# Kernel tuning notes

Hardware: AMD Instinct MI355X
Metric: run time of the kernel (lower is better)

The kernel has to match this reference:

```python
import jax, jax.numpy as jnp
import numpy as np

B, S, E, H = 2, 2048, 768, 8
D = E // H  # 96
SCALING = D ** (-0.5)


def setup_inputs() -> dict:
    key = jax.random.key(0)
    ks = jax.random.split(key, 7)
    sd = E ** -0.5
    return {
        "x": jax.random.normal(ks[0], (B, S, E), jnp.float32),
        "Wq": jax.random.normal(ks[1], (E, E), jnp.float32) * sd,
        "bq": jax.random.normal(ks[2], (E,), jnp.float32) * 0.02,
        "Wk": jax.random.normal(ks[3], (E, E), jnp.float32) * sd,
        "bk": jax.random.normal(ks[4], (E,), jnp.float32) * 0.02,
        "Wo": jax.random.normal(ks[5], (E, E), jnp.float32) * sd,
        "bo": jax.random.normal(ks[6], (E,), jnp.float32) * 0.02,
    }


def _split_heads(t):
    # [B, S, E] -> [B, H, S, D]
    return t.reshape(B, S, H, D).transpose(0, 2, 1, 3)


def reference(x, Wq, bq, Wk, bk, Wo, bo):
    q = _split_heads(x @ Wq + bq)
    k = _split_heads(x @ Wk + bk)
    # NOTE: faithful to source bug — values use the KEY projection
    v = _split_heads(x @ Wk + bk)
    energies = jnp.einsum("bhqd,bhkd->bhqk", q, k)  # [B,H,S,S]
    # NOTE: faithful to source — scaling applied AFTER softmax
    attn = jax.nn.softmax(energies, axis=-1) * SCALING
    out = jnp.einsum("bhqk,bhkd->bhqd", attn, v)
    out = out.transpose(0, 2, 1, 3).reshape(B, S, E)
    return out @ Wo + bo
```

## Files before the change

### kernel.cpp

```cpp
#include <hip/hip_runtime.h>
#include <hip/hip_bf16.h>
#include <math.h>
#include <stdint.h>

#define B_DIM 2
#define S_DIM 2048
#define E_DIM 768
#define H_DIM 8
#define D_DIM 96
#define M_DIM (B_DIM*S_DIM)
#define SCALE_F 0.10206207261596575f
#define LOG2E_F 1.44269504088896341f

typedef _Float16 f16x8 __attribute__((ext_vector_type(8)));
typedef float    f32x4  __attribute__((ext_vector_type(4)));
typedef float    f32x16 __attribute__((ext_vector_type(16)));
typedef unsigned int u32x4 __attribute__((ext_vector_type(4)));

#define MFMA16H(a,b,c) __builtin_amdgcn_mfma_f32_16x16x32_f16(a,b,c,0,0,0)
#define MFMA32H(a,b,c) __builtin_amdgcn_mfma_f32_32x32x16_f16(a,b,c,0,0,0)

__device__ inline unsigned short f2h(float f) {
    return __builtin_bit_cast(unsigned short, (_Float16)f);
}

__device__ inline unsigned pk2(float a, float b) {
    return __builtin_bit_cast(unsigned, __builtin_amdgcn_cvt_pkrtz(a, b));
}

__device__ inline void gload16(const void* g, void* l) {
    auto gp = reinterpret_cast<const __attribute__((address_space(1))) uint32_t*>(
        reinterpret_cast<uintptr_t>(g));
    auto lp = reinterpret_cast<__attribute__((address_space(3))) uint32_t*>(
        reinterpret_cast<uintptr_t>(l));
    __builtin_amdgcn_global_load_lds(gp, lp, 16, 0, 0);
}

__global__ __launch_bounds__(256) void prep_kernel(
    const float* __restrict__ X,
    const float* __restrict__ W0, const float* __restrict__ W1,
    const float* __restrict__ W2,
    unsigned short* __restrict__ Xf,
    unsigned short* __restrict__ T0, unsigned short* __restrict__ T1,
    unsigned short* __restrict__ T2)
{
    const int tid = threadIdx.x;
    if (blockIdx.x < 3072) {
        int i = (blockIdx.x * 256 + tid) * 4;
        float4 v = *(const float4*)(X + i);
        ushort4 h;
        h.x = f2h(v.x); h.y = f2h(v.y); h.z = f2h(v.z); h.w = f2h(v.w);
        *(ushort4*)(Xf + i) = h;
        return;
    }
    int idx = blockIdx.x - 3072;
    int z = idx / 144, rem = idx % 144;
    const float* W; unsigned short* T;
    if (z == 0)      { W = W0; T = T0; }
    else if (z == 1) { W = W1; T = T1; }
    else             { W = W2; T = T2; }
    const float sc = (z == 0) ? LOG2E_F : 1.0f;
    int k0 = (rem / 12) << 6, n0 = (rem % 12) << 6;

    __shared__ float tile[64][65];
    const int r = tid >> 4, c4 = (tid & 15) << 2;
    #pragma unroll
    for (int i = 0; i < 4; ++i) {
        float4 v = *(const float4*)(W + (size_t)(k0 + r + i*16)*E_DIM + n0 + c4);
        tile[r + i*16][c4+0] = v.x; tile[r + i*16][c4+1] = v.y;
        tile[r + i*16][c4+2] = v.z; tile[r + i*16][c4+3] = v.w;
    }
    __syncthreads();
    #pragma unroll
    for (int i = 0; i < 4; ++i) {
        int n = r + i*16;
        ushort4 h;
        h.x = f2h(tile[c4+0][n] * sc); h.y = f2h(tile[c4+1][n] * sc);
        h.z = f2h(tile[c4+2][n] * sc); h.w = f2h(tile[c4+3][n] * sc);
        *(ushort4*)(T + (size_t)(n0 + n)*E_DIM + k0 + c4) = h;
    }
}

__global__ __launch_bounds__(256) void gemm_qk_kernel(
    const unsigned short* __restrict__ A, const unsigned short* __restrict__ Bt,
    const float* __restrict__ bq, const float* __restrict__ bk,
    unsigned short* __restrict__ Qf, unsigned short* __restrict__ Kf)
{
    __shared__ unsigned short sA[2*128*32];
    __shared__ unsigned short sB[2*64*32];

    const int tid  = threadIdx.x;
    const int lane = tid & 63;
    const int w    = tid >> 6;
    const int qn   = lane & 15, quad = lane >> 4;
    const int wm   = w & 1, wn = w >> 1;

    const int flat = blockIdx.x;
    const int g = flat & 7, s = flat >> 3;
    const int row0 = ((g << 2) + (s & 3)) << 7;
    const int col0 = (s >> 2) << 6;

    const int ar = tid >> 2;
    const int ak = (tid & 3) << 3;

    const unsigned short* gA = A  + (size_t)(row0 + ar)*E_DIM + ak;
    const unsigned short* gB = Bt + (size_t)(col0 + ar)*E_DIM + ak;

    f32x4 acc[4][2];
    #pragma unroll
    for (int mt = 0; mt < 4; ++mt)
        #pragma unroll
        for (int nt = 0; nt < 2; ++nt)
            { acc[mt][nt][0]=0.f; acc[mt][nt][1]=0.f; acc[mt][nt][2]=0.f; acc[mt][nt][3]=0.f; }

    for (int k0 = 0; k0 < E_DIM; k0 += 64) {
        __syncthreads();
        gload16(gA + k0,                 sA + tid*8);
        gload16(gA + 64*E_DIM + k0,      sA + 2048 + tid*8);
        gload16(gA + k0 + 32,            sA + 4096 + tid*8);
        gload16(gA + 64*E_DIM + k0 + 32, sA + 6144 + tid*8);
        gload16(gB + k0,                 sB + tid*8);
        gload16(gB + k0 + 32,            sB + 2048 + tid*8);
        __syncthreads();

        #pragma unroll
        for (int kk = 0; kk < 2; ++kk) {
            f16x8 af[4], bf[2];
            #pragma unroll
            for (int mt = 0; mt < 4; ++mt)
                af[mt] = *(const f16x8*)&sA[kk*4096 + (wm*64 + mt*16 + qn)*32 + quad*8];
            #pragma unroll
            for (int nt = 0; nt < 2; ++nt)
                bf[nt] = *(const f16x8*)&sB[kk*2048 + (wn*32 + nt*16 + qn)*32 + quad*8];
            #pragma unroll
            for (int mt = 0; mt < 4; ++mt)
                #pragma unroll
                for (int nt = 0; nt < 2; ++nt)
                    acc[mt][nt] = MFMA16H(af[mt], bf[nt], acc[mt][nt]);
        }
    }

    #pragma unroll
    for (int nt = 0; nt < 2; ++nt) {
        int n = col0 + wn*32 + nt*16 + qn;
        bool isQ = n < E_DIM;
        float bias = isQ ? bq[n] * LOG2E_F : bk[n - E_DIM];
        unsigned short* op = isQ ? Qf : Kf;
        int nc = isQ ? n : n - E_DIM;
        #pragma unroll
        for (int mt = 0; mt < 4; ++mt)
            #pragma unroll
            for (int r = 0; r < 4; ++r) {
                int m = row0 + wm*64 + mt*16 + quad*4 + r;
                op[(size_t)m*E_DIM + nc] = f2h(acc[mt][nt][r] + bias);
            }
    }
}

__global__ __launch_bounds__(256, 3) void attn_mfma_kernel(
    const unsigned short* __restrict__ Qf, const unsigned short* __restrict__ Kf,
    unsigned short* __restrict__ O0, unsigned short* __restrict__ O1,
    unsigned short* __restrict__ O2, unsigned short* __restrict__ O3,
    float2* __restrict__ ml)
{
    __shared__ unsigned short sKh[64][104];
    __shared__ unsigned short sKt[96][72];

    const int tid  = threadIdx.x;
    const int w    = tid >> 6;
    const int lane = tid & 63;
    const int col  = lane & 31;
    const int half = lane >> 5;
    const int b    = blockIdx.z >> 2;
    const int ks   = blockIdx.z & 3;
    const int h    = blockIdx.y;
    const int q0   = blockIdx.x << 7;
    const int key0 = ks << 9;

    f16x8 qf[6];
    {
        const size_t ro = ((size_t)(b*S_DIM + q0 + w*32 + col))*E_DIM
                          + h*D_DIM + half*8;
        #pragma unroll
        for (int kc = 0; kc < 6; ++kc)
            qf[kc] = *(const f16x8*)(Qf + ro + kc*16);
    }

    f32x16 o[3];
    #pragma unroll
    for (int nt = 0; nt < 3; ++nt)
        #pragma unroll
        for (int r = 0; r < 16; ++r) o[nt][r] = 0.f;
    float m_i = -INFINITY, l_i = 0.f;

    const bool stager = tid < 128;
    const int st = tid & 127;
    const int sp = st >> 2;
    const int dq = st & 3;
    const int kp2 = ((sp + ((dq & 1) << 4)) & 31) << 1;

    uint4 r0[3], r1[3];
    if (stager) {
        const size_t g0 = ((size_t)(b*S_DIM + key0 + 2*sp))*E_DIM + h*D_DIM + dq*8;
        #pragma unroll
        for (int i = 0; i < 3; ++i) {
            r0[i] = *(const uint4*)(Kf + g0 + 32*i);
            r1[i] = *(const uint4*)(Kf + g0 + E_DIM + 32*i);
        }
    }

    const int kswz = ((col >> 3) & 1) << 2;

    for (int kt = 0; kt < 8; ++kt) {
        if (stager) {
            #pragma unroll
            for (int i = 0; i < 3; ++i) {
                *(uint4*)&sKh[2*sp  ][dq*8 + 32*i] = r0[i];
                *(uint4*)&sKh[2*sp+1][dq*8 + 32*i] = r1[i];
            }
            const unsigned short* p0 = (const unsigned short*)r0;
            const unsigned short* p1 = (const unsigned short*)r1;
            #pragma unroll
            for (int c = 0; c < 24; ++c) {
                int d = dq*8 + ((c >> 3) << 5) + (c & 7);
                unsigned pk = (unsigned)p0[c] | ((unsigned)p1[c] << 16);
                *(unsigned*)&sKt[d][kp2] = pk;
            }
        }
        __syncthreads();

        if (stager && kt + 1 < 8) {
            const size_t g0 = ((size_t)(b*S_DIM + key0 + (kt+1)*64 + 2*sp))*E_DIM
                              + h*D_DIM + dq*8;
            #pragma unroll
            for (int i = 0; i < 3; ++i) {
                r0[i] = *(const uint4*)(Kf + g0 + 32*i);
                r1[i] = *(const uint4*)(Kf + g0 + E_DIM + 32*i);
            }
        }

        f32x16 s[2];
        #pragma unroll
        for (int mt = 0; mt < 2; ++mt) {
            f32x16 acc;
            #pragma unroll
            for (int r = 0; r < 16; ++r) acc[r] = 0.f;
            #pragma unroll
            for (int kc = 0; kc < 6; ++kc) {
                f16x8 ah = *(const f16x8*)&sKh[mt*32 + col][kc*16 + half*8];
                acc = MFMA32H(ah, qf[kc], acc);
            }
            s[mt] = acc;
        }

        float t[8];
        #pragma unroll
        for (int r = 0; r < 8; ++r)
            t[r] = fmaxf(fmaxf(s[0][r], s[0][r+8]), fmaxf(s[1][r], s[1][r+8]));
        float mx = fmaxf(fmaxf(fmaxf(t[0], t[1]), fmaxf(t[2], t[3])),
                         fmaxf(fmaxf(t[4], t[5]), fmaxf(t[6], t[7])));
        mx = fmaxf(mx, __shfl_xor(mx, 32));

        if (__any(mx > m_i + 10.0f)) {
            float m_new = fmaxf(m_i, mx);
            float alpha = __builtin_amdgcn_exp2f(m_i - m_new);
            l_i *= alpha;
            #pragma unroll
            for (int nt = 0; nt < 3; ++nt)
                #pragma unroll
                for (int r = 0; r < 16; ++r) o[nt][r] *= alpha;
            m_i = m_new;
        }

        #pragma unroll
        for (int mt = 0; mt < 2; ++mt)
            #pragma unroll
            for (int r = 0; r < 16; ++r)
                s[mt][r] = __builtin_amdgcn_exp2f(s[mt][r] - m_i);

        float a[8];
        #pragma unroll
        for (int r = 0; r < 8; ++r)
            a[r] = (s[0][r] + s[0][r+8]) + (s[1][r] + s[1][r+8]);
        float ps = ((a[0]+a[1]) + (a[2]+a[3])) + ((a[4]+a[5]) + (a[6]+a[7]));
        ps += __shfl_xor(ps, 32);
        l_i += ps;

        #pragma unroll
        for (int kc = 0; kc < 4; ++kc) {
            const int mt = kc >> 1;
            const int g0 = (kc & 1) << 3;
            unsigned A0 = pk2(s[mt][g0+0], s[mt][g0+1]);
            unsigned A1 = pk2(s[mt][g0+2], s[mt][g0+3]);
            unsigned B0 = pk2(s[mt][g0+4], s[mt][g0+5]);
            unsigned B1 = pk2(s[mt][g0+6], s[mt][g0+7]);
            auto w0 = __builtin_amdgcn_permlane32_swap(A0, B0, false, false);
            auto w1 = __builtin_amdgcn_permlane32_swap(A1, B1, false, false);
            u32x4 pw;
            pw[0] = w0[0]; pw[1] = w1[0]; pw[2] = w0[1]; pw[3] = w1[1];
            f16x8 pb = __builtin_bit_cast(f16x8, pw);
            #pragma unroll
            for (int nt = 0; nt < 3; ++nt) {
                f16x8 va = *(const f16x8*)
                    &sKt[nt*32 + col][(((kc << 1) | half) ^ kswz) << 3];
                o[nt] = MFMA32H(va, pb, o[nt]);
            }
        }
        __syncthreads();
    }

    float inv = 1.0f / l_i;
    unsigned short* Obase = O0;
    if (ks == 1) Obase = O1; else if (ks == 2) Obase = O2; else if (ks == 3) Obase = O3;
    unsigned short* Ob = Obase
        + ((size_t)(b*S_DIM + q0 + w*32 + col))*E_DIM + h*D_DIM;
    #pragma unroll
    for (int nt = 0; nt < 3; ++nt)
        #pragma unroll
        for (int rg = 0; rg < 4; ++rg) {
            ushort4 pk;
            pk.x = f2h(o[nt][4*rg+0]*inv); pk.y = f2h(o[nt][4*rg+1]*inv);
            pk.z = f2h(o[nt][4*rg+2]*inv); pk.w = f2h(o[nt][4*rg+3]*inv);
            *(ushort4*)(Ob + nt*32 + 8*rg + 4*half) = pk;
        }
    if (lane < 32) {
        int q = q0 + w*32 + lane;
        ml[((size_t)(ks*B_DIM + b)*H_DIM + h)*S_DIM + q] = make_float2(m_i, l_i);
    }
}

__device__ inline float4 mkscale4(const float2* __restrict__ ml, int m, int h) {
    int b = m >> 11, q = m & (S_DIM - 1);
    float2 e0 = ml[((size_t)(0*B_DIM + b)*H_DIM + h)*S_DIM + q];
    float2 e1 = ml[((size_t)(1*B_DIM + b)*H_DIM + h)*S_DIM + q];
    float2 e2 = ml[((size_t)(2*B_DIM + b)*H_DIM + h)*S_DIM + q];
    float2 e3 = ml[((size_t)(3*B_DIM + b)*H_DIM + h)*S_DIM + q];
    float mm = fmaxf(fmaxf(e0.x, e1.x), fmaxf(e2.x, e3.x));
    float w0 = e0.y * __builtin_amdgcn_exp2f(e0.x - mm);
    float w1 = e1.y * __builtin_amdgcn_exp2f(e1.x - mm);
    float w2 = e2.y * __builtin_amdgcn_exp2f(e2.x - mm);
    float w3 = e3.y * __builtin_amdgcn_exp2f(e3.x - mm);
    float inv = SCALE_F / (w0 + w1 + w2 + w3);
    return make_float4(w0*inv, w1*inv, w2*inv, w3*inv);
}

__global__ __launch_bounds__(256) void gemm_out_kernel(
    const unsigned short* __restrict__ O0, const unsigned short* __restrict__ O1,
    const unsigned short* __restrict__ O2, const unsigned short* __restrict__ O3,
    const float2* __restrict__ ml, const unsigned short* __restrict__ Bt,
    const float* __restrict__ bo, float* __restrict__ out)
{
    __shared__ unsigned short sA[2*64*32];
    __shared__ unsigned short sB[2*64*32];

    const int tid  = threadIdx.x;
    const int lane = tid & 63;
    const int w    = tid >> 6;
    const int qn   = lane & 15, quad = lane >> 4;
    const int wm   = w & 1, wn = w >> 1;

    const int flat = blockIdx.x;
    const int g = flat & 7, s = flat >> 3;
    const int row0 = ((g << 3) + (s & 7)) << 6;
    const int col0 = (s >> 3) << 6;

    const int ar = tid >> 2;
    const int ak = (tid & 3) << 3;

    const size_t r0o = (size_t)(row0 + ar)*E_DIM;
    const unsigned short* gB = Bt + (size_t)(col0 + ar)*E_DIM + ak;

    f32x4 acc[2][2];
    #pragma unroll
    for (int mt = 0; mt < 2; ++mt)
        #pragma unroll
        for (int nt = 0; nt < 2; ++nt)
            { acc[mt][nt][0]=0.f; acc[mt][nt][1]=0.f; acc[mt][nt][2]=0.f; acc[mt][nt][3]=0.f; }

    f16x8 u0A = *(const f16x8*)(O0 + r0o + ak);
    f16x8 u1A = *(const f16x8*)(O1 + r0o + ak);
    f16x8 u2A = *(const f16x8*)(O2 + r0o + ak);
    f16x8 u3A = *(const f16x8*)(O3 + r0o + ak);
    f16x8 u0B = *(const f16x8*)(O0 + r0o + 32 + ak);
    f16x8 u1B = *(const f16x8*)(O1 + r0o + 32 + ak);
    f16x8 u2B = *(const f16x8*)(O2 + r0o + 32 + ak);
    f16x8 u3B = *(const f16x8*)(O3 + r0o + 32 + ak);
    int hA = 0, hB = 0;
    float4 s4 = mkscale4(ml, row0 + ar, 0);
    _Float16 aA0 = (_Float16)s4.x, aA1 = (_Float16)s4.y;
    _Float16 aA2 = (_Float16)s4.z, aA3 = (_Float16)s4.w;
    _Float16 aB0 = aA0, aB1 = aA1, aB2 = aA2, aB3 = aA3;

    for (int k0 = 0; k0 < E_DIM; k0 += 64) {
        __syncthreads();
        {
            f16x8 c0 = (u0A*aA0 + u1A*aA1) + (u2A*aA2 + u3A*aA3);
            f16x8 c1 = (u0B*aB0 + u1B*aB1) + (u2B*aB2 + u3B*aB3);
            *(f16x8*)&sA[       ar*32 + ak] = c0;
            *(f16x8*)&sA[2048 + ar*32 + ak] = c1;
        }
        gload16(gB + k0,      sB + tid*8);
        gload16(gB + k0 + 32, sB + 2048 + tid*8);
        __syncthreads();

        if (k0 + 64 < E_DIM) {
            int kn = k0 + 64;
            u0A = *(const f16x8*)(O0 + r0o + kn + ak);
            u1A = *(const f16x8*)(O1 + r0o + kn + ak);
            u2A = *(const f16x8*)(O2 + r0o + kn + ak);
            u3A = *(const f16x8*)(O3 + r0o + kn + ak);
            u0B = *(const f16x8*)(O0 + r0o + kn + 32 + ak);
            u1B = *(const f16x8*)(O1 + r0o + kn + 32 + ak);
            u2B = *(const f16x8*)(O2 + r0o + kn + 32 + ak);
            u3B = *(const f16x8*)(O3 + r0o + kn + 32 + ak);
            int nhA = kn / D_DIM, nhB = (kn + 32) / D_DIM;
            if (nhA != hA) {
                float4 t4 = mkscale4(ml, row0 + ar, nhA);
                aA0 = (_Float16)t4.x; aA1 = (_Float16)t4.y;
                aA2 = (_Float16)t4.z; aA3 = (_Float16)t4.w; hA = nhA;
            }
            if (nhB != hB) {
                float4 t4 = mkscale4(ml, row0 + ar, nhB);
                aB0 = (_Float16)t4.x; aB1 = (_Float16)t4.y;
                aB2 = (_Float16)t4.z; aB3 = (_Float16)t4.w; hB = nhB;
            }
        }

        #pragma unroll
        for (int kk = 0; kk < 2; ++kk) {
            f16x8 af[2], bf[2];
            #pragma unroll
            for (int mt = 0; mt < 2; ++mt)
                af[mt] = *(const f16x8*)&sA[kk*2048 + (wm*32 + mt*16 + qn)*32 + quad*8];
            #pragma unroll
            for (int nt = 0; nt < 2; ++nt)
                bf[nt] = *(const f16x8*)&sB[kk*2048 + (wn*32 + nt*16 + qn)*32 + quad*8];
            #pragma unroll
            for (int mt = 0; mt < 2; ++mt)
                #pragma unroll
                for (int nt = 0; nt < 2; ++nt)
                    acc[mt][nt] = MFMA16H(af[mt], bf[nt], acc[mt][nt]);
        }
    }

    #pragma unroll
    for (int nt = 0; nt < 2; ++nt) {
        int n = col0 + wn*32 + nt*16 + qn;
        float bias = bo[n];
        #pragma unroll
        for (int mt = 0; mt < 2; ++mt)
            #pragma unroll
            for (int r = 0; r < 4; ++r) {
                int m = row0 + wm*32 + mt*16 + quad*4 + r;
                out[(size_t)m*E_DIM + n] = acc[mt][nt][r] + bias;
            }
    }
}

extern "C" void kernel_launch(void* const* d_in, const int* in_sizes, int n_in,
                              void* d_out, int out_size, void* d_ws, size_t ws_size,
                              hipStream_t stream)
{
    const float* x  = (const float*)d_in[0];
    const float* Wq = (const float*)d_in[1];
    const float* bq = (const float*)d_in[2];
    const float* Wk = (const float*)d_in[3];
    const float* bk = (const float*)d_in[4];
    const float* Wo = (const float*)d_in[5];
    const float* bo = (const float*)d_in[6];
    float* out = (float*)d_out;

    const size_t NE = (size_t)M_DIM * E_DIM;
    const size_t WE = (size_t)E_DIM * E_DIM;
    unsigned short* xf    = (unsigned short*)d_ws;
    unsigned short* WqkT  = xf + NE;
    unsigned short* WoT   = WqkT + 2*WE;
    unsigned short* Qf    = WoT + WE;
    unsigned short* Kf    = Qf + NE;
    unsigned short* Oh1   = Kf + NE;
    unsigned short* Oh2   = Oh1 + NE;
    unsigned short* Oh3   = Oh2 + NE;
    float2*         mlbuf = (float2*)(Oh3 + NE);
    unsigned short* Oh0   = xf;

    dim3 blk(256);
    hipLaunchKernelGGL(prep_kernel, dim3(3504), blk, 0, stream,
                       x, Wq, Wk, Wo, xf, WqkT, WqkT + WE, WoT);

    hipLaunchKernelGGL(gemm_qk_kernel, dim3(768), blk, 0, stream,
                       xf, WqkT, bq, bk, Qf, Kf);

    hipLaunchKernelGGL(attn_mfma_kernel, dim3(S_DIM/128, H_DIM, B_DIM*4), blk, 0,
                       stream, Qf, Kf, Oh0, Oh1, Oh2, Oh3, mlbuf);

    hipLaunchKernelGGL(gemm_out_kernel, dim3(768), blk, 0, stream,
                       Oh0, Oh1, Oh2, Oh3, mlbuf, WoT, bo, out);
}
```

Measured before the change: 161.5 us.

## Process two query tiles per wave in attention, halving block size

The attention kernel now runs 128 threads (2 waves) per block instead of 4, and each wave handles 64 query rows as two 32-row sub-tiles. Every K fragment read from shared memory feeds two MFMAs, which halves LDS reads per FLOP, and all threads now take part in staging K. The cost is roughly double the accumulator and score registers per wave (launch bounds relaxed to 2), which lowers occupancy and risks register pressure or spills.

```diff
diff --git a/kernel.cpp b/kernel.cpp
--- a/kernel.cpp
+++ b/kernel.cpp
@@ -157,7 +157,7 @@
     }
 }
 
-__global__ __launch_bounds__(256, 3) void attn_mfma_kernel(
+__global__ __launch_bounds__(128, 2) void attn_mfma_kernel(
     const unsigned short* __restrict__ Qf, const unsigned short* __restrict__ Kf,
     unsigned short* __restrict__ O0, unsigned short* __restrict__ O1,
     unsigned short* __restrict__ O2, unsigned short* __restrict__ O3,
@@ -177,30 +177,32 @@
     const int q0   = blockIdx.x << 7;
     const int key0 = ks << 9;
 
-    f16x8 qf[6];
+    f16x8 qf[2][6];
+    #pragma unroll
+    for (int qb = 0; qb < 2; ++qb) {
+        const size_t ro = ((size_t)(b*S_DIM + q0 + w*64 + qb*32 + col))*E_DIM
+                          + h*D_DIM + half*8;
+        #pragma unroll
+        for (int kc = 0; kc < 6; ++kc)
+            qf[qb][kc] = *(const f16x8*)(Qf + ro + kc*16);
+    }
+
+    f32x16 o[2][3];
+    #pragma unroll
+    for (int qb = 0; qb < 2; ++qb)
+        #pragma unroll
+        for (int nt = 0; nt < 3; ++nt)
+            #pragma unroll
+            for (int r = 0; r < 16; ++r) o[qb][nt][r] = 0.f;
+    float m_i[2] = {-INFINITY, -INFINITY};
+    float l_i[2] = {0.f, 0.f};
+
+    const int sp = tid >> 2;
+    const int dq = tid & 3;
+    const int kp2 = ((sp + ((dq & 1) << 4)) & 31) << 1;
+
+    uint4 r0[3], r1[3];
     {
-        const size_t ro = ((size_t)(b*S_DIM + q0 + w*32 + col))*E_DIM
-                          + h*D_DIM + half*8;
-        #pragma unroll
-        for (int kc = 0; kc < 6; ++kc)
-            qf[kc] = *(const f16x8*)(Qf + ro + kc*16);
-    }
-
-    f32x16 o[3];
-    #pragma unroll
-    for (int nt = 0; nt < 3; ++nt)
-        #pragma unroll
-        for (int r = 0; r < 16; ++r) o[nt][r] = 0.f;
-    float m_i = -INFINITY, l_i = 0.f;
-
-    const bool stager = tid < 128;
-    const int st = tid & 127;
-    const int sp = st >> 2;
-    const int dq = st & 3;
-    const int kp2 = ((sp + ((dq & 1) << 4)) & 31) << 1;
-
-    uint4 r0[3], r1[3];
-    if (stager) {
         const size_t g0 = ((size_t)(b*S_DIM + key0 + 2*sp))*E_DIM + h*D_DIM + dq*8;
         #pragma unroll
         for (int i = 0; i < 3; ++i) {
@@ -212,7 +214,7 @@
     const int kswz = ((col >> 3) & 1) << 2;
 
     for (int kt = 0; kt < 8; ++kt) {
-        if (stager) {
+        {
             #pragma unroll
             for (int i = 0; i < 3; ++i) {
                 *(uint4*)&sKh[2*sp  ][dq*8 + 32*i] = r0[i];
@@ -229,7 +231,7 @@
         }
         __syncthreads();
 
-        if (stager && kt + 1 < 8) {
+        if (kt + 1 < 8) {
             const size_t g0 = ((size_t)(b*S_DIM + key0 + (kt+1)*64 + 2*sp))*E_DIM
                               + h*D_DIM + dq*8;
             #pragma unroll
@@ -239,93 +241,111 @@
             }
         }
 
-        f32x16 s[2];
-        #pragma unroll
-        for (int mt = 0; mt < 2; ++mt) {
-            f32x16 acc;
-            #pragma unroll
-            for (int r = 0; r < 16; ++r) acc[r] = 0.f;
+        f32x16 s[2][2];
+        #pragma unroll
+        for (int qb = 0; qb < 2; ++qb)
+            #pragma unroll
+            for (int mt = 0; mt < 2; ++mt)
+                #pragma unroll
+                for (int r = 0; r < 16; ++r) s[qb][mt][r] = 0.f;
+        #pragma unroll
+        for (int mt = 0; mt < 2; ++mt)
             #pragma unroll
             for (int kc = 0; kc < 6; ++kc) {
                 f16x8 ah = *(const f16x8*)&sKh[mt*32 + col][kc*16 + half*8];
-                acc = MFMA32H(ah, qf[kc], acc);
-            }
-            s[mt] = acc;
-        }
-
-        float t[8];
-        #pragma unroll
-        for (int r = 0; r < 8; ++r)
-            t[r] = fmaxf(fmaxf(s[0][r], s[0][r+8]), fmaxf(s[1][r], s[1][r+8]));
-        float mx = fmaxf(fmaxf(fmaxf(t[0], t[1]), fmaxf(t[2], t[3])),
-                         fmaxf(fmaxf(t[4], t[5]), fmaxf(t[6], t[7])));
-        mx = fmaxf(mx, __shfl_xor(mx, 32));
-
-        if (__any(mx > m_i + 10.0f)) {
-            float m_new = fmaxf(m_i, mx);
-            float alpha = __builtin_amdgcn_exp2f(m_i - m_new);
-            l_i *= alpha;
-            #pragma unroll
-            for (int nt = 0; nt < 3; ++nt)
+                s[0][mt] = MFMA32H(ah, qf[0][kc], s[0][mt]);
+                s[1][mt] = MFMA32H(ah, qf[1][kc], s[1][mt]);
+            }
+
+        #pragma unroll
+        for (int qb = 0; qb < 2; ++qb) {
+            float t[8];
+            #pragma unroll
+            for (int r = 0; r < 8; ++r)
+                t[r] = fmaxf(fmaxf(s[qb][0][r], s[qb][0][r+8]),
+                             fmaxf(s[qb][1][r], s[qb][1][r+8]));
+            float mx = fmaxf(fmaxf(fmaxf(t[0], t[1]), fmaxf(t[2], t[3])),
+                             fmaxf(fmaxf(t[4], t[5]), fmaxf(t[6], t[7])));
+            mx = fmaxf(mx, __shfl_xor(mx, 32));
+
+            if (__any(mx > m_i[qb] + 10.0f)) {
+                float m_new = fmaxf(m_i[qb], mx);
+                float alpha = __builtin_amdgcn_exp2f(m_i[qb] - m_new);
+                l_i[qb] *= alpha;
                 #pragma unroll
-                for (int r = 0; r < 16; ++r) o[nt][r] *= alpha;
-            m_i = m_new;
-        }
-
-        #pragma unroll
-        for (int mt = 0; mt < 2; ++mt)
-            #pragma unroll
-            for (int r = 0; r < 16; ++r)
-                s[mt][r] = __builtin_amdgcn_exp2f(s[mt][r] - m_i);
-
-        float a[8];
-        #pragma unroll
-        for (int r = 0; r < 8; ++r)
-            a[r] = (s[0][r] + s[0][r+8]) + (s[1][r] + s[1][r+8]);
-        float ps = ((a[0]+a[1]) + (a[2]+a[3])) + ((a[4]+a[5]) + (a[6]+a[7]));
-        ps += __shfl_xor(ps, 32);
-        l_i += ps;
+                for (int nt = 0; nt < 3; ++nt)
+                    #pragma unroll
+                    for (int r = 0; r < 16; ++r) o[qb][nt][r] *= alpha;
+                m_i[qb] = m_new;
+            }
+
+            #pragma unroll
+            for (int mt = 0; mt < 2; ++mt)
+                #pragma unroll
+                for (int r = 0; r < 16; ++r)
+                    s[qb][mt][r] = __builtin_amdgcn_exp2f(s[qb][mt][r] - m_i[qb]);
+
+            float a[8];
+            #pragma unroll
+            for (int r = 0; r < 8; ++r)
+                a[r] = (s[qb][0][r] + s[qb][0][r+8]) + (s[qb][1][r] + s[qb][1][r+8]);
+            float ps = ((a[0]+a[1]) + (a[2]+a[3])) + ((a[4]+a[5]) + (a[6]+a[7]));
+            ps += __shfl_xor(ps, 32);
+            l_i[qb] += ps;
+        }
 
         #pragma unroll
         for (int kc = 0; kc < 4; ++kc) {
             const int mt = kc >> 1;
             const int g0 = (kc & 1) << 3;
-            unsigned A0 = pk2(s[mt][g0+0], s[mt][g0+1]);
-            unsigned A1 = pk2(s[mt][g0+2], s[mt][g0+3]);
-            unsigned B0 = pk2(s[mt][g0+4], s[mt][g0+5]);
-            unsigned B1 = pk2(s[mt][g0+6], s[mt][g0+7]);
-            auto w0 = __builtin_amdgcn_permlane32_swap(A0, B0, false, false);
-            auto w1 = __builtin_amdgcn_permlane32_swap(A1, B1, false, false);
-            u32x4 pw;
-            pw[0] = w0[0]; pw[1] = w1[0]; pw[2] = w0[1]; pw[3] = w1[1];
-            f16x8 pb = __builtin_bit_cast(f16x8, pw);
+            f16x8 pb[2];
+            #pragma unroll
+            for (int qb = 0; qb < 2; ++qb) {
+                unsigned A0 = pk2(s[qb][mt][g0+0], s[qb][mt][g0+1]);
+                unsigned A1 = pk2(s[qb][mt][g0+2], s[qb][mt][g0+3]);
+                unsigned B0 = pk2(s[qb][mt][g0+4], s[qb][mt][g0+5]);
+                unsigned B1 = pk2(s[qb][mt][g0+6], s[qb][mt][g0+7]);
+                auto w0 = __builtin_amdgcn_permlane32_swap(A0, B0, false, false);
+                auto w1 = __builtin_amdgcn_permlane32_swap(A1, B1, false, false);
+                u32x4 pw;
+                pw[0] = w0[0]; pw[1] = w1[0]; pw[2] = w0[1]; pw[3] = w1[1];
+                pb[qb] = __builtin_bit_cast(f16x8, pw);
+            }
             #pragma unroll
             for (int nt = 0; nt < 3; ++nt) {
                 f16x8 va = *(const f16x8*)
                     &sKt[nt*32 + col][(((kc << 1) | half) ^ kswz) << 3];
-                o[nt] = MFMA32H(va, pb, o[nt]);
+                o[0][nt] = MFMA32H(va, pb[0], o[0][nt]);
+                o[1][nt] = MFMA32H(va, pb[1], o[1][nt]);
             }
         }
         __syncthreads();
     }
 
-    float inv = 1.0f / l_i;
     unsigned short* Obase = O0;
     if (ks == 1) Obase = O1; else if (ks == 2) Obase = O2; else if (ks == 3) Obase = O3;
-    unsigned short* Ob = Obase
-        + ((size_t)(b*S_DIM + q0 + w*32 + col))*E_DIM + h*D_DIM;
-    #pragma unroll
-    for (int nt = 0; nt < 3; ++nt)
-        #pragma unroll
-        for (int rg = 0; rg < 4; ++rg) {
-            ushort4 pk;
-            pk.x = f2h(o[nt][4*rg+0]*inv); pk.y = f2h(o[nt][4*rg+1]*inv);
-            pk.z = f2h(o[nt][4*rg+2]*inv); pk.w = f2h(o[nt][4*rg+3]*inv);
-            *(ushort4*)(Ob + nt*32 + 8*rg + 4*half) = pk;
-        }
+    #pragma unroll
+    for (int qb = 0; qb < 2; ++qb) {
+        float inv = 1.0f / l_i[qb];
+        unsigned short* Ob = Obase
+            + ((size_t)(b*S_DIM + q0 + w*64 + qb*32 + col))*E_DIM + h*D_DIM;
+        #pragma unroll
+        for (int nt = 0; nt < 3; ++nt)
+            #pragma unroll
+            for (int rg = 0; rg < 4; ++rg) {
+                ushort4 pk;
+                pk.x = f2h(o[qb][nt][4*rg+0]*inv); pk.y = f2h(o[qb][nt][4*rg+1]*inv);
+                pk.z = f2h(o[qb][nt][4*rg+2]*inv); pk.w = f2h(o[qb][nt][4*rg+3]*inv);
+                *(ushort4*)(Ob + nt*32 + 8*rg + 4*half) = pk;
+            }
+    }
     if (lane < 32) {
-        int q = q0 + w*32 + lane;
-        ml[((size_t)(ks*B_DIM + b)*H_DIM + h)*S_DIM + q] = make_float2(m_i, l_i);
+        #pragma unroll
+        for (int qb = 0; qb < 2; ++qb) {
+            int q = q0 + w*64 + qb*32 + lane;
+            ml[((size_t)(ks*B_DIM + b)*H_DIM + h)*S_DIM + q]
+                = make_float2(m_i[qb], l_i[qb]);
+        }
     }
 }
 
@@ -490,8 +510,8 @@
     hipLaunchKernelGGL(gemm_qk_kernel, dim3(768), blk, 0, stream,
                        xf, WqkT, bq, bk, Qf, Kf);
 
-    hipLaunchKernelGGL(attn_mfma_kernel, dim3(S_DIM/128, H_DIM, B_DIM*4), blk, 0,
-                       stream, Qf, Kf, Oh0, Oh1, Oh2, Oh3, mlbuf);
+    hipLaunchKernelGGL(attn_mfma_kernel, dim3(S_DIM/128, H_DIM, B_DIM*4),
+                       dim3(128), 0, stream, Qf, Kf, Oh0, Oh1, Oh2, Oh3, mlbuf);
 
     hipLaunchKernelGGL(gemm_out_kernel, dim3(768), blk, 0, stream,
                        Oh0, Oh1, Oh2, Oh3, mlbuf, WoT, bo, out);
```

After: 162.2 us. Within noise of the previous version (+0.4%).
